# Performance work log

Hardware: AMD Instinct MI355X
Metric: run time of the kernel (lower is better)

The kernel has to match this reference:

```python
import jax, jax.numpy as jnp
import numpy as np

N = 50000      # nodes (single node type 'tx')
E = 400000     # edges per edge type ('fwd' and 'rev')
F_IN = 128     # input feature dim
F = 128        # cfg.gnn.dim_inner
H = 8          # attention heads
D = F // H     # per-head dim
L = 2          # cfg.gnn.layers_mp
C = 2          # dim_out (fraud logits)


def setup_inputs() -> dict:
    key = jax.random.key(0)
    k = jax.random.split(key, 12)
    f32 = jnp.float32
    g = lambda kk, sh, fan: jax.random.normal(kk, sh, f32) / np.float32(np.sqrt(fan))
    return dict(
        x=jax.random.normal(k[0], (N, F_IN), f32),
        edge_index_fwd=jax.random.randint(k[1], (2, E), 0, N),
        edge_index_rev=jax.random.randint(k[2], (2, E), 0, N),
        in_w=g(k[3], (F_IN, F), F_IN),
        in_b=jnp.zeros((F,), f32),
        kqv_w=g(k[4], (L, F, 3 * F), F),
        kqv_b=jnp.zeros((L, 3 * F), f32),
        krel_w=g(k[5], (L, 2, H, D, D), D),
        vrel_w=g(k[6], (L, 2, H, D, D), D),
        p_rel=jnp.ones((L, 2, H), f32),
        out_w=g(k[7], (L, F, F), F),
        out_b=jnp.zeros((L, F), f32),
        skip=jnp.ones((L,), f32),
        head_w=g(k[8], (F, C), F),
        head_b=jnp.zeros((C,), f32),
    )


def reference(x, edge_index_fwd, edge_index_rev, in_w, in_b, kqv_w, kqv_b,
              krel_w, vrel_w, p_rel, out_w, out_b, skip, head_w, head_b):
    n = x.shape[0]
    ef, er = edge_index_fwd, edge_index_rev
    Ef, Er = ef.shape[1], er.shape[1]
    dst = jnp.concatenate([ef[1], er[1]])                 # [E_tot]
    scale = 1.0 / jnp.sqrt(jnp.asarray(D, x.dtype))

    h = x @ in_w + in_b                                   # in_proj['tx'], [N,F]
    for l in range(L):
        kqv = h @ kqv_w[l] + kqv_b[l]                     # [N,3F]
        k, q, v = jnp.split(kqv, 3, axis=1)
        k = k.reshape(n, H, D)
        q = q.reshape(n, H, D)
        v = v.reshape(n, H, D)
        # per-edge-type relation transforms (head-wise DxD, no bias)
        k_rel = jnp.einsum('nhd,ehdf->enhf', k, krel_w[l])  # [2,N,H,D]
        v_rel = jnp.einsum('nhd,ehdf->enhf', v, vrel_w[l])
        # gather src features per edge type, concatenate edge types
        k_j = jnp.concatenate([k_rel[0][ef[0]], k_rel[1][er[0]]], axis=0)  # [E_tot,H,D]
        v_j = jnp.concatenate([v_rel[0][ef[0]], v_rel[1][er[0]]], axis=0)
        p_e = jnp.concatenate([jnp.broadcast_to(p_rel[l, 0], (Ef, H)),
                               jnp.broadcast_to(p_rel[l, 1], (Er, H))], axis=0)
        q_i = q[dst]                                       # [E_tot,H,D]
        alpha = jnp.einsum('ehd,ehd->eh', q_i, k_j) * p_e * scale
        # segment softmax over all incoming edges of each dst node
        m = jax.ops.segment_max(alpha, dst, num_segments=n)
        ex = jnp.exp(alpha - m[dst])
        denom = jax.ops.segment_sum(ex, dst, num_segments=n)
        w = ex / (denom[dst] + 1e-16)                      # [E_tot,H]
        agg = jax.ops.segment_sum(w[:, :, None] * v_j, dst,
                                  num_segments=n).reshape(n, F)
        a = jax.nn.gelu(agg, approximate=False) @ out_w[l] + out_b[l]
        g = jax.nn.sigmoid(skip[l])
        h = jax.nn.relu(g * a + (1.0 - g) * h)             # skip + act(dropout=0)
    return h @ head_w + head_b                             # logits [N,C]
```

## Files before the change

### kernel.cpp

```cpp
#include <hip/hip_runtime.h>
#include <math.h>

typedef short short8 __attribute__((ext_vector_type(8)));
typedef float f32x4 __attribute__((ext_vector_type(4)));

__device__ __forceinline__ unsigned short f2bf(float f){
    unsigned u = __float_as_uint(f);
    unsigned r = u + 0x7fffu + ((u >> 16) & 1u);
    return (unsigned short)(r >> 16);
}

__global__ void k_zero_i(int* __restrict__ p, int n)
{
    for (int i = blockIdx.x*blockDim.x + threadIdx.x; i < n; i += gridDim.x*blockDim.x)
        p[i] = 0;
}

__global__ void k_count(const int* __restrict__ ef, const int* __restrict__ er,
                        int* __restrict__ deg, int Ef, int Er)
{
    int Etot = Ef + Er;
    for (int e = blockIdx.x*blockDim.x + threadIdx.x; e < Etot; e += gridDim.x*blockDim.x) {
        int dst = (e < Ef) ? ef[Ef + e] : er[Er + (e - Ef)];
        atomicAdd(&deg[dst], 1);
    }
}

__global__ void k_chunk_sums(const int* __restrict__ deg, int* __restrict__ csum, int n)
{
    __shared__ int s[256];
    int t = threadIdx.x, i = blockIdx.x*256 + t;
    s[t] = (i < n) ? deg[i] : 0;
    __syncthreads();
    for (int off = 128; off > 0; off >>= 1) {
        if (t < off) s[t] += s[t + off];
        __syncthreads();
    }
    if (t == 0) csum[blockIdx.x] = s[0];
}

__global__ void k_scan_chunks(int* __restrict__ csum, int nch)
{
    __shared__ int s[1024];
    int t = threadIdx.x;
    int v = (t < nch) ? csum[t] : 0;
    s[t] = v; __syncthreads();
    for (int off = 1; off < 1024; off <<= 1) {
        int u = (t >= off) ? s[t - off] : 0;
        __syncthreads();
        s[t] += u;
        __syncthreads();
    }
    if (t < nch) csum[t] = s[t] - v;
}

__global__ void k_rowstart(const int* __restrict__ deg, const int* __restrict__ csum,
                           int* __restrict__ row_start, int* __restrict__ cursor, int n)
{
    __shared__ int s[256];
    int t = threadIdx.x, i = blockIdx.x*256 + t;
    int d = (i < n) ? deg[i] : 0;
    s[t] = d; __syncthreads();
    for (int off = 1; off < 256; off <<= 1) {
        int u = (t >= off) ? s[t - off] : 0;
        __syncthreads();
        s[t] += u;
        __syncthreads();
    }
    if (i <= n) {
        int rs = csum[blockIdx.x] + s[t] - d;
        row_start[i] = rs;
        cursor[i] = rs;
    }
}

__global__ void k_fill(const int* __restrict__ ef, const int* __restrict__ er,
                       int* __restrict__ cursor, unsigned* __restrict__ srcs,
                       int Ef, int Er, int n_nodes)
{
    int Etot = Ef + Er;
    if (blockIdx.x == 0 && threadIdx.x == 0) {
        srcs[Etot] = 0; srcs[Etot + 1] = 0;
    }
    for (int e = blockIdx.x*blockDim.x + threadIdx.x; e < Etot; e += gridDim.x*blockDim.x) {
        int src, dst, tt;
        if (e < Ef) { src = ef[e]; dst = ef[Ef + e]; tt = 0; }
        else { int e2 = e - Ef; src = er[e2]; dst = er[Er + e2]; tt = 1; }
        int pos = atomicAdd(&cursor[dst], 1);
        srcs[pos] = (unsigned)(tt*n_nodes + src)*32u;
    }
}

__global__ void k_compose(const float* __restrict__ kqv_w, const float* __restrict__ kqv_b,
                          const float* __restrict__ krel_w, const float* __restrict__ vrel_w,
                          const float* __restrict__ p_rel, unsigned short* __restrict__ WcT,
                          float* __restrict__ biasc)
{
    int idx = blockIdx.x*blockDim.x + threadIdx.x;
    int tot = 2*129*640;
    if (idx >= tot) return;
    int l = idx / (129*640);
    int rem = idx % (129*640);
    int r = rem / 640, c = rem % 640;
    float val;
    if (c < 128) {
        val = (r < 128) ? kqv_w[((size_t)l*128 + r)*384 + 128 + c]
                        : kqv_b[l*384 + 128 + c];
    } else {
        int c2 = c - 128;
        int tt = c2 >> 8;
        int cc = c2 & 255;
        int f = cc >> 1;
        int part = cc & 1;
        int hh = f >> 4, fd = f & 15;
        const float* rw = (part == 0 ? krel_w : vrel_w)
                          + (((size_t)(l*2 + tt)*8 + hh)*16)*16 + fd;
        int base_col = (part == 0 ? 0 : 256) + hh*16;
        float s = 0.f;
        #pragma unroll
        for (int d = 0; d < 16; ++d) {
            float a = (r < 128) ? kqv_w[((size_t)l*128 + r)*384 + base_col + d]
                                : kqv_b[l*384 + base_col + d];
            s += a * rw[d*16];
        }
        if (part == 0) s *= p_rel[(l*2 + tt)*8 + hh] * 0.25f * 1.4426950408889634f;
        val = s;
    }
    if (r < 128) WcT[((size_t)l*640 + c)*128 + r] = f2bf(val);
    else         biasc[l*640 + c] = val;
}

__global__ void k_compose_out(const float* __restrict__ out_w, const float* __restrict__ out_b,
                              unsigned short* __restrict__ WoT, float* __restrict__ biaso)
{
    int idx = blockIdx.x*blockDim.x + threadIdx.x;
    int tot = 2*129*128;
    if (idx >= tot) return;
    int l = idx / (129*128);
    int rem = idx % (129*128);
    int r = rem / 128, c = rem % 128;
    if (r < 128) WoT[((size_t)l*128 + c)*128 + r] = f2bf(out_w[((size_t)l*128 + r)*128 + c]);
    else         biaso[l*128 + c] = out_b[l*128 + c];
}

__global__ __launch_bounds__(256) void k_mfma(
    const float* __restrict__ A, const unsigned short* __restrict__ WT,
    const float* __restrict__ biasc, float* __restrict__ out0,
    unsigned* __restrict__ kv, const float* __restrict__ skip, int l,
    int n_nodes, int R, int C, int mode)
{
    __shared__ uint4 As[64*16];
    __shared__ uint4 Ws[64*16];
    int b = blockIdx.x;
    int xcd = b & 7, jj = b >> 3;
    int r_t = (jj / C)*8 + xcd;
    int c_t = jj % C;
    if (r_t >= R) return;
    int n0 = r_t*64, c0 = c_t*64;
    int t = threadIdx.x;

    #pragma unroll
    for (int it = 0; it < 4; ++it) {
        int gi = t + it*256;
        int m = gi >> 4, g = gi & 15;
        int n = n0 + m;
        float4 a0 = make_float4(0.f,0.f,0.f,0.f), a1 = a0;
        if (n < n_nodes) {
            a0 = *(const float4*)&A[(size_t)n*128 + g*8];
            a1 = *(const float4*)&A[(size_t)n*128 + g*8 + 4];
        }
        uint4 wd;
        wd.x = (unsigned)f2bf(a0.x) | ((unsigned)f2bf(a0.y) << 16);
        wd.y = (unsigned)f2bf(a0.z) | ((unsigned)f2bf(a0.w) << 16);
        wd.z = (unsigned)f2bf(a1.x) | ((unsigned)f2bf(a1.y) << 16);
        wd.w = (unsigned)f2bf(a1.z) | ((unsigned)f2bf(a1.w) << 16);
        As[m*16 + (g ^ (m & 15))] = wd;
    }
    #pragma unroll
    for (int it = 0; it < 4; ++it) {
        int gi = t + it*256;
        int cw = gi >> 4, g = gi & 15;
        uint4 wv = *(const uint4*)&WT[((size_t)(c0 + cw))*128 + g*8];
        Ws[cw*16 + (g ^ (cw & 15))] = wv;
    }
    __syncthreads();

    int lane = t & 63, w = t >> 6;
    int lm = lane & 15, quad = lane >> 4;
    f32x4 acc[4];
    #pragma unroll
    for (int i = 0; i < 4; ++i) { acc[i][0]=0.f; acc[i][1]=0.f; acc[i][2]=0.f; acc[i][3]=0.f; }

    #pragma unroll
    for (int chunk = 0; chunk < 4; ++chunk) {
        int gq = chunk*4 + quad;
        short8 bfrag = *(const short8*)&Ws[(w*16 + lm)*16 + (gq ^ lm)];
        #pragma unroll
        for (int i = 0; i < 4; ++i) {
            short8 afrag = *(const short8*)&As[(i*16 + lm)*16 + (gq ^ lm)];
            acc[i] = __builtin_amdgcn_mfma_f32_16x16x32_bf16(afrag, bfrag, acc[i], 0, 0, 0);
        }
    }

    int c = c0 + w*16 + lm;
    float bc = biasc[c];
    if (mode == 2) {
        float g = 1.f/(1.f + expf(-skip[l]));
        #pragma unroll
        for (int i = 0; i < 4; ++i) {
            #pragma unroll
            for (int rr = 0; rr < 4; ++rr) {
                int m = n0 + i*16 + quad*4 + rr;
                if (m < n_nodes) {
                    size_t o = (size_t)m*128 + c;
                    float hv = out0[o];
                    out0[o] = fmaxf(g*(acc[i][rr] + bc) + (1.f - g)*hv, 0.f);
                }
            }
        }
    } else if (c0 < 128) {
        #pragma unroll
        for (int i = 0; i < 4; ++i) {
            #pragma unroll
            for (int rr = 0; rr < 4; ++rr) {
                int m = n0 + i*16 + quad*4 + rr;
                if (m < n_nodes) out0[(size_t)m*128 + c] = acc[i][rr] + bc;
            }
        }
    } else {
        int c2 = c - 128;
        int tt = c2 >> 8;
        int f = (c2 & 255) >> 1;
        unsigned* dst = kv + (size_t)tt*n_nodes*128;
        bool isk = (lane & 1) == 0;
        #pragma unroll
        for (int i = 0; i < 4; ++i) {
            #pragma unroll
            for (int rr = 0; rr < 4; ++rr) {
                float val = acc[i][rr] + bc;
                float other = __shfl_xor(val, 1);
                int m = n0 + i*16 + quad*4 + rr;
                if (isk && m < n_nodes) {
                    unsigned wd = ((unsigned)f2bf(val) << 16) | (unsigned)f2bf(other);
                    dst[(size_t)m*128 + f] = wd;
                }
            }
        }
    }
}

__global__ __launch_bounds__(256) void k_gemm(
    const float* __restrict__ A, const float* __restrict__ W, int ldw,
    const float* __restrict__ bias, float* __restrict__ out0,
    int n_nodes, int ncol_tiles)
{
    __shared__ float As_t[32][64];
    __shared__ float Ws[32][64];
    int tile_n = blockIdx.x / ncol_tiles;
    int tile_c = blockIdx.x % ncol_tiles;
    int n0 = tile_n*64, c0 = tile_c*64;
    int t = threadIdx.x, tx = t & 15, ty = t >> 4;

    float4 b4 = *(const float4*)&bias[c0 + tx*4];
    float acc[4][4];
    #pragma unroll
    for (int r = 0; r < 4; ++r) {
        acc[r][0] = b4.x; acc[r][1] = b4.y; acc[r][2] = b4.z; acc[r][3] = b4.w;
    }

    for (int kk = 0; kk < 128; kk += 32) {
        __syncthreads();
        #pragma unroll
        for (int it = 0; it < 2; ++it) {
            int idx = t + it*256;
            int m = idx >> 3, c4 = idx & 7;
            int n = n0 + m;
            float4 a = make_float4(0.f, 0.f, 0.f, 0.f);
            if (n < n_nodes) a = *(const float4*)&A[(size_t)n*128 + kk + c4*4];
            int col = m ^ (c4 << 3);
            As_t[c4*4 + 0][col] = a.x;
            As_t[c4*4 + 1][col] = a.y;
            As_t[c4*4 + 2][col] = a.z;
            As_t[c4*4 + 3][col] = a.w;
        }
        #pragma unroll
        for (int it = 0; it < 2; ++it) {
            int idx = t + it*256;
            int r = idx >> 4, c4 = idx & 15;
            *(float4*)&Ws[r][c4*4] = *(const float4*)&W[(size_t)(kk + r)*ldw + c0 + c4*4];
        }
        __syncthreads();
        #pragma unroll 8
        for (int k = 0; k < 32; ++k) {
            float4 a = *(const float4*)&As_t[k][(ty*4) ^ ((k >> 2) << 3)];
            float4 w = *(const float4*)&Ws[k][tx*4];
            acc[0][0] += a.x*w.x; acc[0][1] += a.x*w.y; acc[0][2] += a.x*w.z; acc[0][3] += a.x*w.w;
            acc[1][0] += a.y*w.x; acc[1][1] += a.y*w.y; acc[1][2] += a.y*w.z; acc[1][3] += a.y*w.w;
            acc[2][0] += a.z*w.x; acc[2][1] += a.z*w.y; acc[2][2] += a.z*w.z; acc[2][3] += a.z*w.w;
            acc[3][0] += a.w*w.x; acc[3][1] += a.w*w.y; acc[3][2] += a.w*w.z; acc[3][3] += a.w*w.w;
        }
    }

    #pragma unroll
    for (int r = 0; r < 4; ++r) {
        int n = n0 + ty*4 + r;
        if (n >= n_nodes) break;
        float4 o = make_float4(acc[r][0], acc[r][1], acc[r][2], acc[r][3]);
        *(float4*)&out0[(size_t)n*128 + c0 + tx*4] = o;
    }
}

__global__ __launch_bounds__(256) void k_attn(
    const unsigned* __restrict__ srcs, const int* __restrict__ row_start,
    const uint4* __restrict__ kv, float* __restrict__ qa, int n_nodes)
{
    int lane = threadIdx.x & 31;
    int n = blockIdx.x*8 + (threadIdx.x >> 5);
    if (n >= n_nodes) return;
    float4 q4 = *(const float4*)&qa[(size_t)n*128 + lane*4];
    int s = row_start[n], e = row_start[n + 1];

    float m0 = -INFINITY, l0 = 0.f; float4 a0 = make_float4(0.f,0.f,0.f,0.f);
    float m1 = -INFINITY, l1 = 0.f; float4 a1 = make_float4(0.f,0.f,0.f,0.f);

    uint4 w0n = kv[srcs[s] + lane];
    uint4 w1n = kv[srcs[s + 1] + lane];
    int pos = s;
    for (; pos + 1 < e; pos += 2) {
        uint4 w0 = w0n, w1 = w1n;
        unsigned sv0 = srcs[pos + 2], sv1 = srcs[pos + 3];
        w0n = kv[sv0 + lane];
        w1n = kv[sv1 + lane];
        float d0 = __uint_as_float(w0.x & 0xffff0000u)*q4.x
                 + __uint_as_float(w0.y & 0xffff0000u)*q4.y
                 + __uint_as_float(w0.z & 0xffff0000u)*q4.z
                 + __uint_as_float(w0.w & 0xffff0000u)*q4.w;
        float d1 = __uint_as_float(w1.x & 0xffff0000u)*q4.x
                 + __uint_as_float(w1.y & 0xffff0000u)*q4.y
                 + __uint_as_float(w1.z & 0xffff0000u)*q4.z
                 + __uint_as_float(w1.w & 0xffff0000u)*q4.w;
        d0 += __shfl_xor(d0, 1); d1 += __shfl_xor(d1, 1);
        d0 += __shfl_xor(d0, 2); d1 += __shfl_xor(d1, 2);
        float mn0 = fmaxf(m0, d0), mn1 = fmaxf(m1, d1);
        float sc0 = exp2f(m0 - mn0), sc1 = exp2f(m1 - mn1);
        float wt0 = exp2f(d0 - mn0), wt1 = exp2f(d1 - mn1);
        l0 = l0*sc0 + wt0;               l1 = l1*sc1 + wt1;
        a0.x = a0.x*sc0 + wt0*__uint_as_float(w0.x << 16);
        a1.x = a1.x*sc1 + wt1*__uint_as_float(w1.x << 16);
        a0.y = a0.y*sc0 + wt0*__uint_as_float(w0.y << 16);
        a1.y = a1.y*sc1 + wt1*__uint_as_float(w1.y << 16);
        a0.z = a0.z*sc0 + wt0*__uint_as_float(w0.z << 16);
        a1.z = a1.z*sc1 + wt1*__uint_as_float(w1.z << 16);
        a0.w = a0.w*sc0 + wt0*__uint_as_float(w0.w << 16);
        a1.w = a1.w*sc1 + wt1*__uint_as_float(w1.w << 16);
        m0 = mn0; m1 = mn1;
    }
    if (pos < e) {
        uint4 w0 = w0n;
        float d = __uint_as_float(w0.x & 0xffff0000u)*q4.x
                + __uint_as_float(w0.y & 0xffff0000u)*q4.y
                + __uint_as_float(w0.z & 0xffff0000u)*q4.z
                + __uint_as_float(w0.w & 0xffff0000u)*q4.w;
        d += __shfl_xor(d, 1);
        d += __shfl_xor(d, 2);
        float mn = fmaxf(m0, d);
        float sc = exp2f(m0 - mn);
        float wt = exp2f(d - mn);
        l0 = l0*sc + wt;
        a0.x = a0.x*sc + wt*__uint_as_float(w0.x << 16);
        a0.y = a0.y*sc + wt*__uint_as_float(w0.y << 16);
        a0.z = a0.z*sc + wt*__uint_as_float(w0.z << 16);
        a0.w = a0.w*sc + wt*__uint_as_float(w0.w << 16);
        m0 = mn;
    }
    float mn = fmaxf(m0, m1);
    float sc0 = (m0 == -INFINITY) ? 0.f : exp2f(m0 - mn);
    float sc1 = (m1 == -INFINITY) ? 0.f : exp2f(m1 - mn);
    float lsum = l0*sc0 + l1*sc1;
    float4 acc;
    acc.x = a0.x*sc0 + a1.x*sc1;
    acc.y = a0.y*sc0 + a1.y*sc1;
    acc.z = a0.z*sc0 + a1.z*sc1;
    acc.w = a0.w*sc0 + a1.w*sc1;

    float inv = 1.f/(lsum + 1e-16f);
    float x0 = acc.x*inv, x1 = acc.y*inv, x2 = acc.z*inv, x3 = acc.w*inv;
    float4 o;
    o.x = 0.5f*x0*(1.f + erff(x0*0.70710678118654752f));
    o.y = 0.5f*x1*(1.f + erff(x1*0.70710678118654752f));
    o.z = 0.5f*x2*(1.f + erff(x2*0.70710678118654752f));
    o.w = 0.5f*x3*(1.f + erff(x3*0.70710678118654752f));
    *(float4*)&qa[(size_t)n*128 + lane*4] = o;
}

__global__ __launch_bounds__(256) void k_head(
    const float* __restrict__ h, const float* __restrict__ hw,
    const float* __restrict__ hb, float* __restrict__ out, int n_nodes)
{
    int n = blockIdx.x*4 + (threadIdx.x >> 6);
    if (n >= n_nodes) return;
    int t = threadIdx.x & 63;
    float h0 = h[(size_t)n*128 + t], h1 = h[(size_t)n*128 + 64 + t];
    float c0 = h0*hw[t*2]     + h1*hw[(t+64)*2];
    float c1 = h0*hw[t*2 + 1] + h1*hw[(t+64)*2 + 1];
    for (int off = 32; off > 0; off >>= 1) {
        c0 += __shfl_down(c0, off);
        c1 += __shfl_down(c1, off);
    }
    if (t == 0) {
        out[n*2]     = c0 + hb[0];
        out[n*2 + 1] = c1 + hb[1];
    }
}

extern "C" void kernel_launch(void* const* d_in, const int* in_sizes, int n_in,
                              void* d_out, int out_size, void* d_ws, size_t ws_size,
                              hipStream_t stream)
{
    const float* x      = (const float*)d_in[0];
    const int*   ef     = (const int*)d_in[1];
    const int*   er     = (const int*)d_in[2];
    const float* in_w   = (const float*)d_in[3];
    const float* in_b   = (const float*)d_in[4];
    const float* kqv_w  = (const float*)d_in[5];
    const float* kqv_b  = (const float*)d_in[6];
    const float* krel_w = (const float*)d_in[7];
    const float* vrel_w = (const float*)d_in[8];
    const float* p_rel  = (const float*)d_in[9];
    const float* out_w  = (const float*)d_in[10];
    const float* out_b  = (const float*)d_in[11];
    const float* skip   = (const float*)d_in[12];
    const float* head_w = (const float*)d_in[13];
    const float* head_b = (const float*)d_in[14];
    float* out = (float*)d_out;

    int n_nodes = in_sizes[0] / 128;
    int Ef = in_sizes[1] / 2, Er = in_sizes[2] / 2;
    int Etot = Ef + Er;
    int nch = (n_nodes + 255)/256;

    float* p = (float*)d_ws;
    float* h    = p; p += (size_t)n_nodes*128;
    float* qa   = p; p += (size_t)n_nodes*128;
    unsigned* kv = (unsigned*)p; p += (size_t)2*n_nodes*128;
    unsigned short* WcT = (unsigned short*)p; p += (size_t)(2*640*128)/2;
    float* biasc = p; p += 2*640;
    unsigned short* WoT = (unsigned short*)p; p += (size_t)(2*128*128)/2;
    float* biaso = p; p += 2*128;
    int* deg       = (int*)p;      p += n_nodes;
    int* csum      = (int*)p;      p += 1024;
    int* row_start = (int*)p;      p += n_nodes + 1;
    int* cursor    = (int*)p;      p += n_nodes + 1;
    unsigned* srcs = (unsigned*)p; p += Etot + 2;

    int ntile = (n_nodes + 63)/64;
    int Rg = (ntile + 7)/8;

    k_zero_i<<<(n_nodes + 255)/256, 256, 0, stream>>>(deg, n_nodes);
    k_count<<<1024, 256, 0, stream>>>(ef, er, deg, Ef, Er);
    k_chunk_sums<<<nch, 256, 0, stream>>>(deg, csum, n_nodes);
    k_scan_chunks<<<1, 1024, 0, stream>>>(csum, nch);
    k_rowstart<<<(n_nodes + 256)/256, 256, 0, stream>>>(deg, csum, row_start, cursor, n_nodes);
    k_fill<<<1024, 256, 0, stream>>>(ef, er, cursor, srcs, Ef, Er, n_nodes);
    k_compose<<<(2*129*640 + 255)/256, 256, 0, stream>>>(kqv_w, kqv_b, krel_w, vrel_w,
                                                         p_rel, WcT, biasc);
    k_compose_out<<<(2*129*128 + 255)/256, 256, 0, stream>>>(out_w, out_b, WoT, biaso);

    k_gemm<<<ntile*2, 256, 0, stream>>>(x, in_w, 128, in_b, h, n_nodes, 2);
    for (int l = 0; l < 2; ++l) {
        k_mfma<<<Rg*8*10, 256, 0, stream>>>(h, WcT + (size_t)l*640*128,
                                            biasc + l*640, qa, kv, skip, l,
                                            n_nodes, ntile, 10, 1);
        k_attn<<<(n_nodes + 7)/8, 256, 0, stream>>>(srcs, row_start,
                                                    (const uint4*)kv, qa, n_nodes);
        k_mfma<<<Rg*8*2, 256, 0, stream>>>(qa, WoT + (size_t)l*128*128,
                                           biaso + l*128, h, kv, skip, l,
                                           n_nodes, ntile, 2, 2);
    }
    k_head<<<(n_nodes + 3)/4, 256, 0, stream>>>(h, head_w, head_b, out, n_nodes);
}
```

Measured before the change: 479.7 us.

## Keep bf16 activation copies and feed MFMA fragments directly from global memory

```diff
diff --git a/kernel.cpp b/kernel.cpp
--- a/kernel.cpp
+++ b/kernel.cpp
@@ -79,9 +79,7 @@
                        int Ef, int Er, int n_nodes)
 {
     int Etot = Ef + Er;
-    if (blockIdx.x == 0 && threadIdx.x == 0) {
-        srcs[Etot] = 0; srcs[Etot + 1] = 0;
-    }
+    if (blockIdx.x == 0 && threadIdx.x == 0) { srcs[Etot] = 0; srcs[Etot + 1] = 0; }
     for (int e = blockIdx.x*blockDim.x + threadIdx.x; e < Etot; e += gridDim.x*blockDim.x) {
         int src, dst, tt;
         if (e < Ef) { src = ef[e]; dst = ef[Ef + e]; tt = 0; }
@@ -89,6 +87,27 @@
         int pos = atomicAdd(&cursor[dst], 1);
         srcs[pos] = (unsigned)(tt*n_nodes + src)*32u;
     }
+}
+
+__global__ void k_cast(const float* __restrict__ src, unsigned short* __restrict__ dst,
+                       long long n)
+{
+    for (long long i = (long long)blockIdx.x*blockDim.x + threadIdx.x; i*4 < n;
+         i += (long long)gridDim.x*blockDim.x) {
+        float4 v = *(const float4*)&src[i*4];
+        uint2 w;
+        w.x = (unsigned)f2bf(v.x) | ((unsigned)f2bf(v.y) << 16);
+        w.y = (unsigned)f2bf(v.z) | ((unsigned)f2bf(v.w) << 16);
+        *(uint2*)&dst[i*4] = w;
+    }
+}
+
+__global__ void k_wt(const float* __restrict__ Wf, unsigned short* __restrict__ WT, int C)
+{
+    int idx = blockIdx.x*blockDim.x + threadIdx.x;
+    if (idx >= 128*C) return;
+    int r = idx / C, c = idx % C;
+    WT[(size_t)c*128 + r] = f2bf(Wf[(size_t)r*C + c]);
 }
 
 __global__ void k_compose(const float* __restrict__ kqv_w, const float* __restrict__ kqv_b,
@@ -144,13 +163,12 @@
 }
 
 __global__ __launch_bounds__(256) void k_mfma(
-    const float* __restrict__ A, const unsigned short* __restrict__ WT,
-    const float* __restrict__ biasc, float* __restrict__ out0,
-    unsigned* __restrict__ kv, const float* __restrict__ skip, int l,
+    const unsigned short* __restrict__ A16, const unsigned short* __restrict__ WT,
+    const float* __restrict__ biasc, float* __restrict__ out_f,
+    unsigned short* __restrict__ out_b16, unsigned* __restrict__ kv,
+    const float* __restrict__ skip, int l,
     int n_nodes, int R, int C, int mode)
 {
-    __shared__ uint4 As[64*16];
-    __shared__ uint4 Ws[64*16];
     int b = blockIdx.x;
     int xcd = b & 7, jj = b >> 3;
     int r_t = (jj / C)*8 + xcd;
@@ -158,46 +176,22 @@
     if (r_t >= R) return;
     int n0 = r_t*64, c0 = c_t*64;
     int t = threadIdx.x;
-
-    #pragma unroll
-    for (int it = 0; it < 4; ++it) {
-        int gi = t + it*256;
-        int m = gi >> 4, g = gi & 15;
-        int n = n0 + m;
-        float4 a0 = make_float4(0.f,0.f,0.f,0.f), a1 = a0;
-        if (n < n_nodes) {
-            a0 = *(const float4*)&A[(size_t)n*128 + g*8];
-            a1 = *(const float4*)&A[(size_t)n*128 + g*8 + 4];
-        }
-        uint4 wd;
-        wd.x = (unsigned)f2bf(a0.x) | ((unsigned)f2bf(a0.y) << 16);
-        wd.y = (unsigned)f2bf(a0.z) | ((unsigned)f2bf(a0.w) << 16);
-        wd.z = (unsigned)f2bf(a1.x) | ((unsigned)f2bf(a1.y) << 16);
-        wd.w = (unsigned)f2bf(a1.z) | ((unsigned)f2bf(a1.w) << 16);
-        As[m*16 + (g ^ (m & 15))] = wd;
-    }
-    #pragma unroll
-    for (int it = 0; it < 4; ++it) {
-        int gi = t + it*256;
-        int cw = gi >> 4, g = gi & 15;
-        uint4 wv = *(const uint4*)&WT[((size_t)(c0 + cw))*128 + g*8];
-        Ws[cw*16 + (g ^ (cw & 15))] = wv;
-    }
-    __syncthreads();
-
     int lane = t & 63, w = t >> 6;
     int lm = lane & 15, quad = lane >> 4;
+
+    const unsigned short* Ab = A16 + (size_t)(n0 + lm)*128 + quad*8;
+    const unsigned short* Bb = WT + (size_t)(c0 + w*16 + lm)*128 + quad*8;
+
     f32x4 acc[4];
     #pragma unroll
     for (int i = 0; i < 4; ++i) { acc[i][0]=0.f; acc[i][1]=0.f; acc[i][2]=0.f; acc[i][3]=0.f; }
 
     #pragma unroll
     for (int chunk = 0; chunk < 4; ++chunk) {
-        int gq = chunk*4 + quad;
-        short8 bfrag = *(const short8*)&Ws[(w*16 + lm)*16 + (gq ^ lm)];
+        short8 bfrag = *(const short8*)(Bb + chunk*32);
         #pragma unroll
         for (int i = 0; i < 4; ++i) {
-            short8 afrag = *(const short8*)&As[(i*16 + lm)*16 + (gq ^ lm)];
+            short8 afrag = *(const short8*)(Ab + (size_t)i*16*128 + chunk*32);
             acc[i] = __builtin_amdgcn_mfma_f32_16x16x32_bf16(afrag, bfrag, acc[i], 0, 0, 0);
         }
     }
@@ -213,18 +207,34 @@
                 int m = n0 + i*16 + quad*4 + rr;
                 if (m < n_nodes) {
                     size_t o = (size_t)m*128 + c;
-                    float hv = out0[o];
-                    out0[o] = fmaxf(g*(acc[i][rr] + bc) + (1.f - g)*hv, 0.f);
+                    float hv = out_f[o];
+                    float nv = fmaxf(g*(acc[i][rr] + bc) + (1.f - g)*hv, 0.f);
+                    out_f[o] = nv;
+                    out_b16[o] = f2bf(nv);
                 }
             }
         }
-    } else if (c0 < 128) {
+    } else if (mode == 0) {
         #pragma unroll
         for (int i = 0; i < 4; ++i) {
             #pragma unroll
             for (int rr = 0; rr < 4; ++rr) {
                 int m = n0 + i*16 + quad*4 + rr;
-                if (m < n_nodes) out0[(size_t)m*128 + c] = acc[i][rr] + bc;
+                if (m < n_nodes) {
+                    size_t o = (size_t)m*128 + c;
+                    float nv = acc[i][rr] + bc;
+                    out_f[o] = nv;
+                    out_b16[o] = f2bf(nv);
+                }
+            }
+        }
+    } else if (c0 < 128) {
+        #pragma unroll
+        for (int i = 0; i < 4; ++i) {
+            #pragma unroll
+            for (int rr = 0; rr < 4; ++rr) {
+                int m = n0 + i*16 + quad*4 + rr;
+                if (m < n_nodes) out_f[(size_t)m*128 + c] = acc[i][rr] + bc;
             }
         }
     } else {
@@ -249,70 +259,10 @@
     }
 }
 
-__global__ __launch_bounds__(256) void k_gemm(
-    const float* __restrict__ A, const float* __restrict__ W, int ldw,
-    const float* __restrict__ bias, float* __restrict__ out0,
-    int n_nodes, int ncol_tiles)
-{
-    __shared__ float As_t[32][64];
-    __shared__ float Ws[32][64];
-    int tile_n = blockIdx.x / ncol_tiles;
-    int tile_c = blockIdx.x % ncol_tiles;
-    int n0 = tile_n*64, c0 = tile_c*64;
-    int t = threadIdx.x, tx = t & 15, ty = t >> 4;
-
-    float4 b4 = *(const float4*)&bias[c0 + tx*4];
-    float acc[4][4];
-    #pragma unroll
-    for (int r = 0; r < 4; ++r) {
-        acc[r][0] = b4.x; acc[r][1] = b4.y; acc[r][2] = b4.z; acc[r][3] = b4.w;
-    }
-
-    for (int kk = 0; kk < 128; kk += 32) {
-        __syncthreads();
-        #pragma unroll
-        for (int it = 0; it < 2; ++it) {
-            int idx = t + it*256;
-            int m = idx >> 3, c4 = idx & 7;
-            int n = n0 + m;
-            float4 a = make_float4(0.f, 0.f, 0.f, 0.f);
-            if (n < n_nodes) a = *(const float4*)&A[(size_t)n*128 + kk + c4*4];
-            int col = m ^ (c4 << 3);
-            As_t[c4*4 + 0][col] = a.x;
-            As_t[c4*4 + 1][col] = a.y;
-            As_t[c4*4 + 2][col] = a.z;
-            As_t[c4*4 + 3][col] = a.w;
-        }
-        #pragma unroll
-        for (int it = 0; it < 2; ++it) {
-            int idx = t + it*256;
-            int r = idx >> 4, c4 = idx & 15;
-            *(float4*)&Ws[r][c4*4] = *(const float4*)&W[(size_t)(kk + r)*ldw + c0 + c4*4];
-        }
-        __syncthreads();
-        #pragma unroll 8
-        for (int k = 0; k < 32; ++k) {
-            float4 a = *(const float4*)&As_t[k][(ty*4) ^ ((k >> 2) << 3)];
-            float4 w = *(const float4*)&Ws[k][tx*4];
-            acc[0][0] += a.x*w.x; acc[0][1] += a.x*w.y; acc[0][2] += a.x*w.z; acc[0][3] += a.x*w.w;
-            acc[1][0] += a.y*w.x; acc[1][1] += a.y*w.y; acc[1][2] += a.y*w.z; acc[1][3] += a.y*w.w;
-            acc[2][0] += a.z*w.x; acc[2][1] += a.z*w.y; acc[2][2] += a.z*w.z; acc[2][3] += a.z*w.w;
-            acc[3][0] += a.w*w.x; acc[3][1] += a.w*w.y; acc[3][2] += a.w*w.z; acc[3][3] += a.w*w.w;
-        }
-    }
-
-    #pragma unroll
-    for (int r = 0; r < 4; ++r) {
-        int n = n0 + ty*4 + r;
-        if (n >= n_nodes) break;
-        float4 o = make_float4(acc[r][0], acc[r][1], acc[r][2], acc[r][3]);
-        *(float4*)&out0[(size_t)n*128 + c0 + tx*4] = o;
-    }
-}
-
 __global__ __launch_bounds__(256) void k_attn(
     const unsigned* __restrict__ srcs, const int* __restrict__ row_start,
-    const uint4* __restrict__ kv, float* __restrict__ qa, int n_nodes)
+    const uint4* __restrict__ kv, const float* __restrict__ qa,
+    unsigned short* __restrict__ qa16, int n_nodes)
 {
     int lane = threadIdx.x & 31;
     int n = blockIdx.x*8 + (threadIdx.x >> 5);
@@ -385,12 +335,14 @@
 
     float inv = 1.f/(lsum + 1e-16f);
     float x0 = acc.x*inv, x1 = acc.y*inv, x2 = acc.z*inv, x3 = acc.w*inv;
-    float4 o;
-    o.x = 0.5f*x0*(1.f + erff(x0*0.70710678118654752f));
-    o.y = 0.5f*x1*(1.f + erff(x1*0.70710678118654752f));
-    o.z = 0.5f*x2*(1.f + erff(x2*0.70710678118654752f));
-    o.w = 0.5f*x3*(1.f + erff(x3*0.70710678118654752f));
-    *(float4*)&qa[(size_t)n*128 + lane*4] = o;
+    float g0 = 0.5f*x0*(1.f + erff(x0*0.70710678118654752f));
+    float g1 = 0.5f*x1*(1.f + erff(x1*0.70710678118654752f));
+    float g2 = 0.5f*x2*(1.f + erff(x2*0.70710678118654752f));
+    float g3 = 0.5f*x3*(1.f + erff(x3*0.70710678118654752f));
+    uint2 pk;
+    pk.x = (unsigned)f2bf(g0) | ((unsigned)f2bf(g1) << 16);
+    pk.y = (unsigned)f2bf(g2) | ((unsigned)f2bf(g3) << 16);
+    *(uint2*)&qa16[(size_t)n*128 + lane*4] = pk;
 }
 
 __global__ __launch_bounds__(256) void k_head(
@@ -438,11 +390,17 @@
     int Ef = in_sizes[1] / 2, Er = in_sizes[2] / 2;
     int Etot = Ef + Er;
     int nch = (n_nodes + 255)/256;
+    int ntile = (n_nodes + 63)/64;
+    int npad = ntile*64;
 
     float* p = (float*)d_ws;
-    float* h    = p; p += (size_t)n_nodes*128;
-    float* qa   = p; p += (size_t)n_nodes*128;
+    float* h    = p; p += (size_t)npad*128;
+    float* qa   = p; p += (size_t)npad*128;
     unsigned* kv = (unsigned*)p; p += (size_t)2*n_nodes*128;
+    unsigned short* h16  = (unsigned short*)p; p += (size_t)npad*128/2;
+    unsigned short* qa16 = (unsigned short*)p; p += (size_t)npad*128/2;
+    unsigned short* x16  = (unsigned short*)p; p += (size_t)npad*128/2;
+    unsigned short* WiT = (unsigned short*)p; p += (size_t)(128*128)/2;
     unsigned short* WcT = (unsigned short*)p; p += (size_t)(2*640*128)/2;
     float* biasc = p; p += 2*640;
     unsigned short* WoT = (unsigned short*)p; p += (size_t)(2*128*128)/2;
@@ -453,7 +411,6 @@
     int* cursor    = (int*)p;      p += n_nodes + 1;
     unsigned* srcs = (unsigned*)p; p += Etot + 2;
 
-    int ntile = (n_nodes + 63)/64;
     int Rg = (ntile + 7)/8;
 
     k_zero_i<<<(n_nodes + 255)/256, 256, 0, stream>>>(deg, n_nodes);
@@ -465,16 +422,19 @@
     k_compose<<<(2*129*640 + 255)/256, 256, 0, stream>>>(kqv_w, kqv_b, krel_w, vrel_w,
                                                          p_rel, WcT, biasc);
     k_compose_out<<<(2*129*128 + 255)/256, 256, 0, stream>>>(out_w, out_b, WoT, biaso);
-
-    k_gemm<<<ntile*2, 256, 0, stream>>>(x, in_w, 128, in_b, h, n_nodes, 2);
+    k_wt<<<(128*128 + 255)/256, 256, 0, stream>>>(in_w, WiT, 128);
+    k_cast<<<2048, 256, 0, stream>>>(x, x16, (long long)n_nodes*128);
+
+    k_mfma<<<Rg*8*2, 256, 0, stream>>>(x16, WiT, in_b, h, h16, kv, skip, 0,
+                                       n_nodes, ntile, 2, 0);
     for (int l = 0; l < 2; ++l) {
-        k_mfma<<<Rg*8*10, 256, 0, stream>>>(h, WcT + (size_t)l*640*128,
-                                            biasc + l*640, qa, kv, skip, l,
+        k_mfma<<<Rg*8*10, 256, 0, stream>>>(h16, WcT + (size_t)l*640*128,
+                                            biasc + l*640, qa, nullptr, kv, skip, l,
                                             n_nodes, ntile, 10, 1);
         k_attn<<<(n_nodes + 7)/8, 256, 0, stream>>>(srcs, row_start,
-                                                    (const uint4*)kv, qa, n_nodes);
-        k_mfma<<<Rg*8*2, 256, 0, stream>>>(qa, WoT + (size_t)l*128*128,
-                                           biaso + l*128, h, kv, skip, l,
+                                                    (const uint4*)kv, qa, qa16, n_nodes);
+        k_mfma<<<Rg*8*2, 256, 0, stream>>>(qa16, WoT + (size_t)l*128*128,
+                                           biaso + l*128, h, h16, kv, skip, l,
                                            n_nodes, ntile, 2, 2);
     }
     k_head<<<(n_nodes + 3)/4, 256, 0, stream>>>(h, head_w, head_b, out, n_nodes);
```

Measured after the change: 575.8 us. 1.2x slower.
